# Kernel optimization log

Measured on AMD Instinct MI355X. Metric: run time of the kernel, lower is better.

Reference implementation:

```python
import jax, jax.numpy as jnp
import numpy as np

B, S, DIM, H = 2, 2048, 512, 8
DEPTH = DIM // H


def setup_inputs() -> dict:
    key = jax.random.key(0)
    ks = jax.random.split(key, 6)
    scale = 1.0 / np.sqrt(DIM)
    X = jax.random.normal(ks[0], (B, S, DIM), dtype=jnp.float32)
    mask = jax.random.randint(ks[1], (B, S), 0, 2).astype(jnp.float32)
    Wq = jax.random.normal(ks[2], (DIM, DIM), dtype=jnp.float32) * scale
    Wk = jax.random.normal(ks[3], (DIM, DIM), dtype=jnp.float32) * scale
    Wv = jax.random.normal(ks[4], (DIM, DIM), dtype=jnp.float32) * scale
    Wo = jax.random.normal(ks[5], (DIM, DIM), dtype=jnp.float32) * scale
    z = jnp.zeros((DIM,), dtype=jnp.float32)
    return {"X": X, "mask": mask, "Wq": Wq, "bq": z, "Wk": Wk, "bk": z,
            "Wv": Wv, "bv": z, "Wo": Wo, "bo": z}


def _split_heads(t):
    # [B, S, DIM] -> [B, H, S, DEPTH]
    return t.reshape(B, S, H, DEPTH).transpose(0, 2, 1, 3)


def reference(X, mask, Wq, bq, Wk, bk, Wv, bv, Wo, bo):
    Q = _split_heads(X @ Wq + bq)
    K = _split_heads(X @ Wk + bk)
    V = _split_heads(X @ Wv + bv)
    # logits: [B, H, Sq, Sk]
    logits = jnp.einsum('bhqd,bhkd->bhqk', Q, K) / jnp.sqrt(jnp.float32(DEPTH))
    logits = logits + mask[:, None, None, :] * (-1e9)
    attn = jax.nn.softmax(logits, axis=-1)
    ctx = jnp.einsum('bhqk,bhkd->bhqd', attn, V)  # [B, H, S, DEPTH]
    concat = ctx.transpose(0, 2, 1, 3).reshape(B, S, DIM)
    out = concat @ Wo + bo
    return (out, attn)
```

## Files before the change

### kernel.cpp

```cpp
#include <hip/hip_runtime.h>
#include <cmath>

#define NB 2
#define SEQ 2048
#define DIM 512
#define NH 8
#define DEPTH 64
#define NT (SEQ / 64)

typedef _Float16 f16_t;
typedef _Float16 f16x4 __attribute__((ext_vector_type(4)));
typedef _Float16 f16x8 __attribute__((ext_vector_type(8)));
typedef float f32x4 __attribute__((ext_vector_type(4)));

#define MFMA16(a, b, c) __builtin_amdgcn_mfma_f32_16x16x32_f16((a), (b), (c), 0, 0, 0)

#define LDS_BARRIER() do { \
    asm volatile("s_waitcnt lgkmcnt(0)\n\ts_barrier" ::: "memory"); \
    __builtin_amdgcn_sched_barrier(0); \
} while (0)

__global__ __launch_bounds__(256) void prep_kernel(
    const float* __restrict__ X,
    const float* __restrict__ Wq, const float* __restrict__ Wk,
    const float* __restrict__ Wv, const float* __restrict__ Wo,
    f16_t* __restrict__ wt, f16_t* __restrict__ wot, f16_t* __restrict__ xh)
{
    const int bx = blockIdx.x;
    if (bx >= 256) {
        const size_t i = ((size_t)(bx - 256) * 256 + threadIdx.x) * 8;
        const f32x4 a = *(const f32x4*)(X + i);
        const f32x4 b = *(const f32x4*)(X + i + 4);
        f16x8 o;
        #pragma unroll
        for (int j = 0; j < 4; ++j) { o[j] = (f16_t)a[j]; o[j+4] = (f16_t)b[j]; }
        *(f16x8*)(xh + i) = o;
        return;
    }
    __shared__ float Ws[64][68];
    const int z  = bx >> 6;
    const int kt = (bx >> 3) & 7;
    const int nt = bx & 7;
    const float* W = (z == 0) ? Wq : (z == 1) ? Wk : (z == 2) ? Wv : Wo;
    const int k0 = kt * 64, n0 = nt * 64;
    const int t = threadIdx.x;
    {
        const int r = t >> 2, c0 = (t & 3) * 16;
        #pragma unroll
        for (int j = 0; j < 4; ++j)
            *(f32x4*)&Ws[r][c0 + j*4] =
                *(const f32x4*)&W[(size_t)(k0 + r) * DIM + n0 + c0 + j*4];
    }
    __syncthreads();
    const int n = t >> 2, kc = (t & 3) * 16;
    f16x8 b0, b1;
    #pragma unroll
    for (int j = 0; j < 8; ++j) {
        b0[j] = (f16_t)Ws[kc + j][n];
        b1[j] = (f16_t)Ws[kc + 8 + j][n];
    }
    f16_t* dst = (z < 3) ? (wt + ((size_t)(z * DIM + n0 + n)) * DIM + k0 + kc)
                         : (wot + (size_t)(n0 + n) * DIM + k0 + kc);
    *(f16x8*)dst = b0;
    *(f16x8*)(dst + 8) = b1;
}

__global__ __launch_bounds__(256, 2) void qkv_gemm_kernel(
    const f16_t* __restrict__ xh, const f16_t* __restrict__ wt,
    const float* __restrict__ bq, const float* __restrict__ bk,
    const float* __restrict__ bv,
    f16_t* __restrict__ q_h, f16_t* __restrict__ k_h, f16_t* __restrict__ v_t)
{
    const int bx = blockIdx.x;
    const int mb = bx & 31, nb = bx >> 5;
    const int tid = threadIdx.x;
    const int w = tid >> 6, lane = tid & 63, l15 = lane & 15, g4 = lane >> 4;
    const int mBase = mb * 128 + (w >> 1) * 64;
    const int nBase = nb * 128 + (w & 1) * 64;

    f32x4 acc[4][4];
    #pragma unroll
    for (int i = 0; i < 4; ++i)
        #pragma unroll
        for (int j = 0; j < 4; ++j) acc[i][j] = (f32x4){0.f, 0.f, 0.f, 0.f};

    for (int k0 = 0; k0 < DIM; k0 += 64) {
        f16x8 ah[4][2];
        #pragma unroll
        for (int mt = 0; mt < 4; ++mt) {
            const f16_t* xr = xh + (size_t)(mBase + mt*16 + l15) * DIM + k0 + g4*8;
            ah[mt][0] = *(const f16x8*)xr;
            ah[mt][1] = *(const f16x8*)(xr + 32);
        }
        #pragma unroll
        for (int nt = 0; nt < 4; ++nt) {
            const f16_t* wr = wt + (size_t)(nBase + nt*16 + l15) * DIM + k0 + g4*8;
            #pragma unroll
            for (int kk = 0; kk < 2; ++kk) {
                f16x8 bw = *(const f16x8*)(wr + kk*32);
                #pragma unroll
                for (int mt = 0; mt < 4; ++mt)
                    acc[mt][nt] = MFMA16(ah[mt][kk], bw, acc[mt][nt]);
            }
        }
    }

    const int z = nb >> 2;
    const float* bias = (z == 0) ? bq : (z == 1) ? bk : bv;
    #pragma unroll
    for (int mt = 0; mt < 4; ++mt) {
        #pragma unroll
        for (int nt = 0; nt < 4; ++nt) {
            const int n = nBase + nt*16 + l15;
            const int col = n & 511;
            const int h = (n >> 6) & 7, d = n & 63;
            const float bb = bias[col];
            #pragma unroll
            for (int r = 0; r < 4; ++r) {
                const int m = mBase + mt*16 + g4*4 + r;
                const int b = m >> 11, s = m & (SEQ - 1);
                const int bh = b * NH + h;
                const float v = acc[mt][nt][r] + bb;
                if (z == 2) {
                    v_t[((size_t)bh * DEPTH + d) * SEQ + s] = (f16_t)v;
                } else {
                    const size_t o = ((size_t)bh * SEQ + s) * DEPTH + d;
                    if (z == 0) q_h[o] = (f16_t)v;
                    else        k_h[o] = (f16_t)v;
                }
            }
        }
    }
}

__global__ __launch_bounds__(256, 3) void attn_kernel(
    const f16_t* __restrict__ q_h, const f16_t* __restrict__ k_h,
    const f16_t* __restrict__ v_t, const float* __restrict__ mask,
    float* __restrict__ attn, f16_t* __restrict__ ctxf)
{
    __shared__ __align__(16) unsigned char smem[46080];
    f16_t (*Kh)[64][72] = (f16_t(*)[64][72])smem;
    f16_t (*Vt)[64][72] = (f16_t(*)[64][72])(smem + 18432);
    f16_t (*Ph)[16][72] = (f16_t(*)[16][72])(smem + 36864);
    float (*cx)[68]     = (float(*)[68])smem;

    const int tid = threadIdx.x;
    const int w = tid >> 6, lane = tid & 63;
    const int l15 = lane & 15, g4 = lane >> 4;
    const int rr = tid >> 2, cc = (tid & 3) << 4;

    const int id  = blockIdx.x;
    const int nid = (id & 7) * 64 + (id >> 3);
    const int bh = nid >> 5, qt = nid & 31;
    const int b = bh >> 3, h = bh & 7;

    const size_t kvb = (size_t)bh * SEQ * DEPTH;
    const f16_t* khp = k_h + kvb;
    const f16_t* vtp = v_t + kvb;
    const float* mp  = mask + b * SEQ;
    float* attn_p = attn + (size_t)bh * SEQ * SEQ;

    const int qb = qt * 64;
    const int qw = qb + w * 16;

    f16x8 qf0, qf1;
    {
        const f16_t* qr = q_h + kvb + (size_t)(qw + l15) * DEPTH + g4 * 8;
        qf0 = *(const f16x8*)qr;
        qf1 = *(const f16x8*)(qr + 32);
    }

    float l_r = 0.f;

    {
        const f16_t* s0 = khp + (size_t)rr * DEPTH + cc;
        *(uint4*)&Kh[0][rr][cc]     = *(const uint4*)s0;
        *(uint4*)&Kh[0][rr][cc + 8] = *(const uint4*)(s0 + 8);
    }
    LDS_BARRIER();

    int cur = 0;
    for (int kt = 0; kt < NT; ++kt) {
        const int kbase = kt * 64;
        f32x4 mb[4];
        #pragma unroll
        for (int nt = 0; nt < 4; ++nt)
            mb[nt] = *(const f32x4*)(mp + kbase + nt*16 + g4*4);

        const bool have = (kt + 1) < NT;
        uint4 nk0, nk1;
        if (have) {
            const f16_t* src = khp + (size_t)((kt+1)*64 + rr) * DEPTH + cc;
            nk0 = *(const uint4*)src;
            nk1 = *(const uint4*)(src + 8);
        }

        float ts = 0.f;
        #pragma unroll
        for (int nt = 0; nt < 4; ++nt) {
            const f16x8 a0 = *(const f16x8*)&Kh[cur][nt*16 + l15][g4*8];
            const f16x8 a1 = *(const f16x8*)&Kh[cur][nt*16 + l15][32 + g4*8];
            __builtin_amdgcn_s_setprio(1);
            f32x4 c = {0.f, 0.f, 0.f, 0.f};
            c = MFMA16(a0, qf0, c);
            c = MFMA16(a1, qf1, c);
            __builtin_amdgcn_s_setprio(0);
            #pragma unroll
            for (int r = 0; r < 4; ++r)
                ts += __expf(c[r] * 0.125f + mb[nt][r] * (-1e9f));
        }
        ts += __shfl_xor(ts, 16);
        ts += __shfl_xor(ts, 32);
        l_r += ts;

        if (have) {
            *(uint4*)&Kh[cur ^ 1][rr][cc]     = nk0;
            *(uint4*)&Kh[cur ^ 1][rr][cc + 8] = nk1;
        }
        LDS_BARRIER();
        cur ^= 1;
    }
    const float invl = 1.0f / l_r;

    f32x4 cacc[4];
    #pragma unroll
    for (int nt = 0; nt < 4; ++nt) cacc[nt] = (f32x4){0.f, 0.f, 0.f, 0.f};

    {
        const f16_t* s0 = khp + (size_t)rr * DEPTH + cc;
        *(uint4*)&Kh[0][rr][cc]     = *(const uint4*)s0;
        *(uint4*)&Kh[0][rr][cc + 8] = *(const uint4*)(s0 + 8);
        const f16_t* s1 = vtp + (size_t)rr * SEQ + cc;
        *(uint4*)&Vt[0][rr][cc]     = *(const uint4*)s1;
        *(uint4*)&Vt[0][rr][cc + 8] = *(const uint4*)(s1 + 8);
    }
    LDS_BARRIER();

    cur = 0;
    for (int kt = 0; kt < NT; ++kt) {
        const int kbase = kt * 64;
        f32x4 mb[4];
        #pragma unroll
        for (int nt = 0; nt < 4; ++nt)
            mb[nt] = *(const f32x4*)(mp + kbase + nt*16 + g4*4);

        const bool have = (kt + 1) < NT;
        uint4 nk0, nk1, nv0, nv1;
        if (have) {
            const f16_t* srck = khp + (size_t)(kbase + 64 + rr) * DEPTH + cc;
            nk0 = *(const uint4*)srck;
            nk1 = *(const uint4*)(srck + 8);
            const f16_t* srcv = vtp + (size_t)rr * SEQ + kbase + 64 + cc;
            nv0 = *(const uint4*)srcv;
            nv1 = *(const uint4*)(srcv + 8);
        }

        #pragma unroll
        for (int nt = 0; nt < 4; ++nt) {
            const f16x8 a0 = *(const f16x8*)&Kh[cur][nt*16 + l15][g4*8];
            const f16x8 a1 = *(const f16x8*)&Kh[cur][nt*16 + l15][32 + g4*8];
            __builtin_amdgcn_s_setprio(1);
            f32x4 c = {0.f, 0.f, 0.f, 0.f};
            c = MFMA16(a0, qf0, c);
            c = MFMA16(a1, qf1, c);
            __builtin_amdgcn_s_setprio(0);
            f32x4 pv;
            f16x4 pc;
            #pragma unroll
            for (int r = 0; r < 4; ++r) {
                pv[r] = __expf(c[r] * 0.125f + mb[nt][r] * (-1e9f)) * invl;
                pc[r] = (f16_t)pv[r];
            }
            __builtin_nontemporal_store(
                pv, (f32x4*)(attn_p + (size_t)(qw + l15) * SEQ + kbase + nt*16 + g4*4));
            *(f16x4*)&Ph[w][l15][nt*16 + g4*4] = pc;
        }
        asm volatile("s_waitcnt lgkmcnt(0)" ::: "memory");
        __builtin_amdgcn_sched_barrier(0);

        #pragma unroll
        for (int kk = 0; kk < 2; ++kk) {
            const f16x8 pf = *(const f16x8*)&Ph[w][l15][kk*32 + g4*8];
            __builtin_amdgcn_s_setprio(1);
            #pragma unroll
            for (int nt = 0; nt < 4; ++nt) {
                const f16x8 vf = *(const f16x8*)&Vt[cur][nt*16 + l15][kk*32 + g4*8];
                cacc[nt] = MFMA16(vf, pf, cacc[nt]);
            }
            __builtin_amdgcn_s_setprio(0);
        }

        if (have) {
            *(uint4*)&Kh[cur ^ 1][rr][cc]     = nk0;
            *(uint4*)&Kh[cur ^ 1][rr][cc + 8] = nk1;
            *(uint4*)&Vt[cur ^ 1][rr][cc]     = nv0;
            *(uint4*)&Vt[cur ^ 1][rr][cc + 8] = nv1;
        }
        LDS_BARRIER();
        cur ^= 1;
    }

    #pragma unroll
    for (int nt = 0; nt < 4; ++nt)
        #pragma unroll
        for (int r = 0; r < 4; ++r)
            cx[nt*16 + g4*4 + r][w*16 + l15] = cacc[nt][r];
    asm volatile("s_waitcnt lgkmcnt(0)" ::: "memory");
    __builtin_amdgcn_sched_barrier(0);
    {
        const int q = tid >> 2, dc = (tid & 3) << 4;
        f16x8 o0, o1;
        #pragma unroll
        for (int j = 0; j < 8; ++j) {
            o0[j] = (f16_t)cx[dc + j][q];
            o1[j] = (f16_t)cx[dc + 8 + j][q];
        }
        f16_t* dst = ctxf + ((size_t)(b * SEQ) + qb + q) * DIM + h * 64 + dc;
        *(f16x8*)dst = o0;
        *(f16x8*)(dst + 8) = o1;
    }
}

__global__ __launch_bounds__(256, 2) void out_gemm_kernel(
    const f16_t* __restrict__ ctxf, const f16_t* __restrict__ wot,
    const float* __restrict__ bo, float* __restrict__ out)
{
    const int bx = blockIdx.x;
    const int mb = bx & 63, nb = bx >> 6;
    const int tid = threadIdx.x;
    const int w = tid >> 6, lane = tid & 63, l15 = lane & 15, g4 = lane >> 4;
    const int mBase = mb * 64 + (w >> 1) * 32;
    const int nBase = nb * 128 + (w & 1) * 64;

    f32x4 acc[2][4];
    #pragma unroll
    for (int i = 0; i < 2; ++i)
        #pragma unroll
        for (int j = 0; j < 4; ++j) acc[i][j] = (f32x4){0.f, 0.f, 0.f, 0.f};

    for (int k0 = 0; k0 < DIM; k0 += 64) {
        f16x8 ah[2][2];
        #pragma unroll
        for (int mt = 0; mt < 2; ++mt) {
            const f16_t* ar = ctxf + (size_t)(mBase + mt*16 + l15) * DIM + k0 + g4*8;
            ah[mt][0] = *(const f16x8*)ar;
            ah[mt][1] = *(const f16x8*)(ar + 32);
        }
        #pragma unroll
        for (int nt = 0; nt < 4; ++nt) {
            const f16_t* wr = wot + (size_t)(nBase + nt*16 + l15) * DIM + k0 + g4*8;
            #pragma unroll
            for (int kk = 0; kk < 2; ++kk) {
                f16x8 bw = *(const f16x8*)(wr + kk*32);
                #pragma unroll
                for (int mt = 0; mt < 2; ++mt)
                    acc[mt][nt] = MFMA16(ah[mt][kk], bw, acc[mt][nt]);
            }
        }
    }
    #pragma unroll
    for (int mt = 0; mt < 2; ++mt) {
        #pragma unroll
        for (int nt = 0; nt < 4; ++nt) {
            const int n = nBase + nt*16 + l15;
            const float bn = bo[n];
            #pragma unroll
            for (int r = 0; r < 4; ++r) {
                const int m = mBase + mt*16 + g4*4 + r;
                out[(size_t)m * DIM + n] = acc[mt][nt][r] + bn;
            }
        }
    }
}

extern "C" void kernel_launch(void* const* d_in, const int* in_sizes, int n_in,
                              void* d_out, int out_size, void* d_ws, size_t ws_size,
                              hipStream_t stream)
{
    const float* X    = (const float*)d_in[0];
    const float* mask = (const float*)d_in[1];
    const float* Wq   = (const float*)d_in[2];
    const float* bq   = (const float*)d_in[3];
    const float* Wk   = (const float*)d_in[4];
    const float* bk   = (const float*)d_in[5];
    const float* Wv   = (const float*)d_in[6];
    const float* bv   = (const float*)d_in[7];
    const float* Wo   = (const float*)d_in[8];
    const float* bo   = (const float*)d_in[9];

    float* out  = (float*)d_out;
    float* attn = out + (size_t)NB * SEQ * DIM;

    const size_t N = (size_t)NB * NH * SEQ * DEPTH;
    f16_t* q_h  = (f16_t*)d_ws;
    f16_t* k_h  = q_h + N;
    f16_t* v_t  = k_h + N;
    f16_t* wt   = v_t + N;
    f16_t* wot  = wt + (size_t)3 * DIM * DIM;
    f16_t* ctxf = wot + (size_t)DIM * DIM;
    f16_t* xh   = ctxf + N;

    prep_kernel<<<1280, 256, 0, stream>>>(X, Wq, Wk, Wv, Wo, wt, wot, xh);

    qkv_gemm_kernel<<<384, 256, 0, stream>>>(xh, wt, bq, bk, bv, q_h, k_h, v_t);

    attn_kernel<<<512, 256, 0, stream>>>(q_h, k_h, v_t, mask, attn, ctxf);

    out_gemm_kernel<<<256, 256, 0, stream>>>(ctxf, wot, bo, out);
}
```

Before: 184.6 us.

## Split attention into row-sum kernel and PV kernel with unrolled double buffering

Moves the first pass (softmax denominator) into a separate kernel with lower LDS use and a higher occupancy bound, and stores 1/l to a workspace buffer. The PV kernel reads that value instead of recomputing it, and both loops are unrolled by two with static buffer indices and prefetched mask loads. Row-sum reduction shuffles move out of the loop. The cost is an extra launch plus a small global round-trip for linv, in exchange for better occupancy and less per-iteration overhead.

```diff
diff --git a/kernel.cpp b/kernel.cpp
--- a/kernel.cpp
+++ b/kernel.cpp
@@ -133,9 +133,113 @@
     }
 }
 
-__global__ __launch_bounds__(256, 3) void attn_kernel(
+__global__ __launch_bounds__(256, 4) void attn_l_kernel(
+    const f16_t* __restrict__ q_h, const f16_t* __restrict__ k_h,
+    const float* __restrict__ mask, float* __restrict__ linv)
+{
+    __shared__ __align__(16) f16_t Kh[2][64][72];
+
+    const int tid = threadIdx.x;
+    const int w = tid >> 6, lane = tid & 63;
+    const int l15 = lane & 15, g4 = lane >> 4;
+    const int rr = tid >> 2, cc = (tid & 3) << 4;
+
+    const int id  = blockIdx.x;
+    const int nid = (id & 7) * 64 + (id >> 3);
+    const int bh = nid >> 5, qt = nid & 31;
+    const int b = bh >> 3;
+
+    const size_t kvb = (size_t)bh * SEQ * DEPTH;
+    const f16_t* khp = k_h + kvb;
+    const float* mp  = mask + b * SEQ;
+    const int qw = qt * 64 + w * 16;
+
+    f16x8 qf0, qf1;
+    {
+        const f16_t* qr = q_h + kvb + (size_t)(qw + l15) * DEPTH + g4 * 8;
+        qf0 = *(const f16x8*)qr;
+        qf1 = *(const f16x8*)(qr + 32);
+    }
+
+    f32x4 mb0[4], mb1[4];
+    float l_r = 0.f;
+
+    {
+        const f16_t* s0 = khp + (size_t)rr * DEPTH + cc;
+        *(uint4*)&Kh[0][rr][cc]     = *(const uint4*)s0;
+        *(uint4*)&Kh[0][rr][cc + 8] = *(const uint4*)(s0 + 8);
+    }
+    #pragma unroll
+    for (int nt = 0; nt < 4; ++nt)
+        mb0[nt] = *(const f32x4*)(mp + nt*16 + g4*4);
+    LDS_BARRIER();
+
+    for (int kt = 0; kt < NT; kt += 2) {
+        uint4 a, b2;
+        #pragma unroll
+        for (int nt = 0; nt < 4; ++nt)
+            mb1[nt] = *(const f32x4*)(mp + (kt+1)*64 + nt*16 + g4*4);
+        {
+            const f16_t* src = khp + (size_t)((kt+1)*64 + rr) * DEPTH + cc;
+            a  = *(const uint4*)src;
+            b2 = *(const uint4*)(src + 8);
+        }
+        #pragma unroll
+        for (int nt = 0; nt < 4; ++nt) {
+            const f16x8 a0 = *(const f16x8*)&Kh[0][nt*16 + l15][g4*8];
+            const f16x8 a1 = *(const f16x8*)&Kh[0][nt*16 + l15][32 + g4*8];
+            __builtin_amdgcn_s_setprio(1);
+            f32x4 c = {0.f, 0.f, 0.f, 0.f};
+            c = MFMA16(a0, qf0, c);
+            c = MFMA16(a1, qf1, c);
+            __builtin_amdgcn_s_setprio(0);
+            #pragma unroll
+            for (int r = 0; r < 4; ++r)
+                l_r += __expf(c[r] * 0.125f + mb0[nt][r] * (-1e9f));
+        }
+        *(uint4*)&Kh[1][rr][cc]     = a;
+        *(uint4*)&Kh[1][rr][cc + 8] = b2;
+        LDS_BARRIER();
+
+        const bool more = (kt + 2) < NT;
+        if (more) {
+            #pragma unroll
+            for (int nt = 0; nt < 4; ++nt)
+                mb0[nt] = *(const f32x4*)(mp + (kt+2)*64 + nt*16 + g4*4);
+            const f16_t* src = khp + (size_t)((kt+2)*64 + rr) * DEPTH + cc;
+            a  = *(const uint4*)src;
+            b2 = *(const uint4*)(src + 8);
+        }
+        #pragma unroll
+        for (int nt = 0; nt < 4; ++nt) {
+            const f16x8 a0 = *(const f16x8*)&Kh[1][nt*16 + l15][g4*8];
+            const f16x8 a1 = *(const f16x8*)&Kh[1][nt*16 + l15][32 + g4*8];
+            __builtin_amdgcn_s_setprio(1);
+            f32x4 c = {0.f, 0.f, 0.f, 0.f};
+            c = MFMA16(a0, qf0, c);
+            c = MFMA16(a1, qf1, c);
+            __builtin_amdgcn_s_setprio(0);
+            #pragma unroll
+            for (int r = 0; r < 4; ++r)
+                l_r += __expf(c[r] * 0.125f + mb1[nt][r] * (-1e9f));
+        }
+        if (more) {
+            *(uint4*)&Kh[0][rr][cc]     = a;
+            *(uint4*)&Kh[0][rr][cc + 8] = b2;
+        }
+        LDS_BARRIER();
+    }
+
+    l_r += __shfl_xor(l_r, 16);
+    l_r += __shfl_xor(l_r, 32);
+    if (lane < 16)
+        linv[(size_t)bh * SEQ + qw + lane] = 1.0f / l_r;
+}
+
+__global__ __launch_bounds__(256, 3) void attn_pv_kernel(
     const f16_t* __restrict__ q_h, const f16_t* __restrict__ k_h,
     const f16_t* __restrict__ v_t, const float* __restrict__ mask,
+    const float* __restrict__ linv,
     float* __restrict__ attn, f16_t* __restrict__ ctxf)
 {
     __shared__ __align__(16) unsigned char smem[46080];
@@ -163,6 +267,8 @@
     const int qb = qt * 64;
     const int qw = qb + w * 16;
 
+    const float invl = linv[(size_t)bh * SEQ + qw + l15];
+
     f16x8 qf0, qf1;
     {
         const f16_t* qr = q_h + kvb + (size_t)(qw + l15) * DEPTH + g4 * 8;
@@ -170,95 +276,17 @@
         qf1 = *(const f16x8*)(qr + 32);
     }
 
-    float l_r = 0.f;
-
-    {
-        const f16_t* s0 = khp + (size_t)rr * DEPTH + cc;
-        *(uint4*)&Kh[0][rr][cc]     = *(const uint4*)s0;
-        *(uint4*)&Kh[0][rr][cc + 8] = *(const uint4*)(s0 + 8);
-    }
-    LDS_BARRIER();
-
-    int cur = 0;
-    for (int kt = 0; kt < NT; ++kt) {
-        const int kbase = kt * 64;
-        f32x4 mb[4];
-        #pragma unroll
-        for (int nt = 0; nt < 4; ++nt)
-            mb[nt] = *(const f32x4*)(mp + kbase + nt*16 + g4*4);
-
-        const bool have = (kt + 1) < NT;
-        uint4 nk0, nk1;
-        if (have) {
-            const f16_t* src = khp + (size_t)((kt+1)*64 + rr) * DEPTH + cc;
-            nk0 = *(const uint4*)src;
-            nk1 = *(const uint4*)(src + 8);
-        }
-
-        float ts = 0.f;
-        #pragma unroll
-        for (int nt = 0; nt < 4; ++nt) {
-            const f16x8 a0 = *(const f16x8*)&Kh[cur][nt*16 + l15][g4*8];
-            const f16x8 a1 = *(const f16x8*)&Kh[cur][nt*16 + l15][32 + g4*8];
-            __builtin_amdgcn_s_setprio(1);
-            f32x4 c = {0.f, 0.f, 0.f, 0.f};
-            c = MFMA16(a0, qf0, c);
-            c = MFMA16(a1, qf1, c);
-            __builtin_amdgcn_s_setprio(0);
-            #pragma unroll
-            for (int r = 0; r < 4; ++r)
-                ts += __expf(c[r] * 0.125f + mb[nt][r] * (-1e9f));
-        }
-        ts += __shfl_xor(ts, 16);
-        ts += __shfl_xor(ts, 32);
-        l_r += ts;
-
-        if (have) {
-            *(uint4*)&Kh[cur ^ 1][rr][cc]     = nk0;
-            *(uint4*)&Kh[cur ^ 1][rr][cc + 8] = nk1;
-        }
-        LDS_BARRIER();
-        cur ^= 1;
-    }
-    const float invl = 1.0f / l_r;
-
     f32x4 cacc[4];
     #pragma unroll
     for (int nt = 0; nt < 4; ++nt) cacc[nt] = (f32x4){0.f, 0.f, 0.f, 0.f};
 
-    {
-        const f16_t* s0 = khp + (size_t)rr * DEPTH + cc;
-        *(uint4*)&Kh[0][rr][cc]     = *(const uint4*)s0;
-        *(uint4*)&Kh[0][rr][cc + 8] = *(const uint4*)(s0 + 8);
-        const f16_t* s1 = vtp + (size_t)rr * SEQ + cc;
-        *(uint4*)&Vt[0][rr][cc]     = *(const uint4*)s1;
-        *(uint4*)&Vt[0][rr][cc + 8] = *(const uint4*)(s1 + 8);
-    }
-    LDS_BARRIER();
-
-    cur = 0;
-    for (int kt = 0; kt < NT; ++kt) {
-        const int kbase = kt * 64;
-        f32x4 mb[4];
-        #pragma unroll
-        for (int nt = 0; nt < 4; ++nt)
-            mb[nt] = *(const f32x4*)(mp + kbase + nt*16 + g4*4);
-
-        const bool have = (kt + 1) < NT;
-        uint4 nk0, nk1, nv0, nv1;
-        if (have) {
-            const f16_t* srck = khp + (size_t)(kbase + 64 + rr) * DEPTH + cc;
-            nk0 = *(const uint4*)srck;
-            nk1 = *(const uint4*)(srck + 8);
-            const f16_t* srcv = vtp + (size_t)rr * SEQ + kbase + 64 + cc;
-            nv0 = *(const uint4*)srcv;
-            nv1 = *(const uint4*)(srcv + 8);
-        }
-
-        #pragma unroll
-        for (int nt = 0; nt < 4; ++nt) {
-            const f16x8 a0 = *(const f16x8*)&Kh[cur][nt*16 + l15][g4*8];
-            const f16x8 a1 = *(const f16x8*)&Kh[cur][nt*16 + l15][32 + g4*8];
+    f32x4 mb0[4], mb1[4];
+
+    auto tile = [&](int buf, const f32x4 (&mb)[4], int kbase) {
+        #pragma unroll
+        for (int nt = 0; nt < 4; ++nt) {
+            const f16x8 a0 = *(const f16x8*)&Kh[buf][nt*16 + l15][g4*8];
+            const f16x8 a1 = *(const f16x8*)&Kh[buf][nt*16 + l15][32 + g4*8];
             __builtin_amdgcn_s_setprio(1);
             f32x4 c = {0.f, 0.f, 0.f, 0.f};
             c = MFMA16(a0, qf0, c);
@@ -277,27 +305,72 @@
         }
         asm volatile("s_waitcnt lgkmcnt(0)" ::: "memory");
         __builtin_amdgcn_sched_barrier(0);
-
         #pragma unroll
         for (int kk = 0; kk < 2; ++kk) {
             const f16x8 pf = *(const f16x8*)&Ph[w][l15][kk*32 + g4*8];
             __builtin_amdgcn_s_setprio(1);
             #pragma unroll
             for (int nt = 0; nt < 4; ++nt) {
-                const f16x8 vf = *(const f16x8*)&Vt[cur][nt*16 + l15][kk*32 + g4*8];
+                const f16x8 vf = *(const f16x8*)&Vt[buf][nt*16 + l15][kk*32 + g4*8];
                 cacc[nt] = MFMA16(vf, pf, cacc[nt]);
             }
             __builtin_amdgcn_s_setprio(0);
         }
-
-        if (have) {
-            *(uint4*)&Kh[cur ^ 1][rr][cc]     = nk0;
-            *(uint4*)&Kh[cur ^ 1][rr][cc + 8] = nk1;
-            *(uint4*)&Vt[cur ^ 1][rr][cc]     = nv0;
-            *(uint4*)&Vt[cur ^ 1][rr][cc + 8] = nv1;
-        }
+    };
+
+    {
+        const f16_t* s0 = khp + (size_t)rr * DEPTH + cc;
+        *(uint4*)&Kh[0][rr][cc]     = *(const uint4*)s0;
+        *(uint4*)&Kh[0][rr][cc + 8] = *(const uint4*)(s0 + 8);
+        const f16_t* s1 = vtp + (size_t)rr * SEQ + cc;
+        *(uint4*)&Vt[0][rr][cc]     = *(const uint4*)s1;
+        *(uint4*)&Vt[0][rr][cc + 8] = *(const uint4*)(s1 + 8);
+    }
+    #pragma unroll
+    for (int nt = 0; nt < 4; ++nt)
+        mb0[nt] = *(const f32x4*)(mp + nt*16 + g4*4);
+    LDS_BARRIER();
+
+    for (int kt = 0; kt < NT; kt += 2) {
+        uint4 nk0, nk1, nv0, nv1;
+        #pragma unroll
+        for (int nt = 0; nt < 4; ++nt)
+            mb1[nt] = *(const f32x4*)(mp + (kt+1)*64 + nt*16 + g4*4);
+        {
+            const f16_t* srck = khp + (size_t)((kt+1)*64 + rr) * DEPTH + cc;
+            nk0 = *(const uint4*)srck;
+            nk1 = *(const uint4*)(srck + 8);
+            const f16_t* srcv = vtp + (size_t)rr * SEQ + (kt+1)*64 + cc;
+            nv0 = *(const uint4*)srcv;
+            nv1 = *(const uint4*)(srcv + 8);
+        }
+        tile(0, mb0, kt * 64);
+        *(uint4*)&Kh[1][rr][cc]     = nk0;
+        *(uint4*)&Kh[1][rr][cc + 8] = nk1;
+        *(uint4*)&Vt[1][rr][cc]     = nv0;
+        *(uint4*)&Vt[1][rr][cc + 8] = nv1;
         LDS_BARRIER();
-        cur ^= 1;
+
+        const bool more = (kt + 2) < NT;
+        if (more) {
+            #pragma unroll
+            for (int nt = 0; nt < 4; ++nt)
+                mb0[nt] = *(const f32x4*)(mp + (kt+2)*64 + nt*16 + g4*4);
+            const f16_t* srck = khp + (size_t)((kt+2)*64 + rr) * DEPTH + cc;
+            nk0 = *(const uint4*)srck;
+            nk1 = *(const uint4*)(srck + 8);
+            const f16_t* srcv = vtp + (size_t)rr * SEQ + (kt+2)*64 + cc;
+            nv0 = *(const uint4*)srcv;
+            nv1 = *(const uint4*)(srcv + 8);
+        }
+        tile(1, mb1, (kt + 1) * 64);
+        if (more) {
+            *(uint4*)&Kh[0][rr][cc]     = nk0;
+            *(uint4*)&Kh[0][rr][cc + 8] = nk1;
+            *(uint4*)&Vt[0][rr][cc]     = nv0;
+            *(uint4*)&Vt[0][rr][cc + 8] = nv1;
+        }
+        LDS_BARRIER();
     }
 
     #pragma unroll
@@ -399,12 +472,15 @@
     f16_t* wot  = wt + (size_t)3 * DIM * DIM;
     f16_t* ctxf = wot + (size_t)DIM * DIM;
     f16_t* xh   = ctxf + N;
+    float* linv = (float*)(xh + N);
 
     prep_kernel<<<1280, 256, 0, stream>>>(X, Wq, Wk, Wv, Wo, wt, wot, xh);
 
     qkv_gemm_kernel<<<384, 256, 0, stream>>>(xh, wt, bq, bk, bv, q_h, k_h, v_t);
 
-    attn_kernel<<<512, 256, 0, stream>>>(q_h, k_h, v_t, mask, attn, ctxf);
+    attn_l_kernel<<<512, 256, 0, stream>>>(q_h, k_h, mask, linv);
+
+    attn_pv_kernel<<<512, 256, 0, stream>>>(q_h, k_h, v_t, mask, linv, attn, ctxf);
 
     out_gemm_kernel<<<256, 256, 0, stream>>>(ctxf, wot, bo, out);
 }
```

New measurement: 178.0 us. -3.6%, faster.
